# Optimization experiments

Measured on AMD Instinct MI355X. Metric: run time of the kernel, lower is better.

The kernel has to match this reference:

```python
import jax, jax.numpy as jnp
import numpy as np

NUM_HEADS = 8
HEAD_SIZE = 64
N_EMBEDS = 512


def setup_inputs() -> dict:
    key = jax.random.key(0)
    kx, kq, kk, kv, kw, kb = jax.random.split(key, 6)
    B, T, C = 8, 2048, N_EMBEDS
    H, D = NUM_HEADS, HEAD_SIZE
    s = 1.0 / np.sqrt(C)
    x = jax.random.normal(kx, (B, T, C), dtype=jnp.float32)
    Wq = jax.random.normal(kq, (H, C, D), dtype=jnp.float32) * s
    Wk = jax.random.normal(kk, (H, C, D), dtype=jnp.float32) * s
    Wv = jax.random.normal(kv, (H, C, D), dtype=jnp.float32) * s
    Wproj = jax.random.normal(kw, (H * D, C), dtype=jnp.float32) * (1.0 / np.sqrt(H * D))
    bproj = jnp.zeros((C,), dtype=jnp.float32)
    return {"x": x, "Wq": Wq, "Wk": Wk, "Wv": Wv, "Wproj": Wproj, "bproj": bproj}


def reference(x, Wq, Wk, Wv, Wproj, bproj):
    # x: [B,T,C]; Wq/Wk/Wv: [H,C,D]; Wproj: [H*D,C]; bproj: [C]
    B, T, C = x.shape
    H, _, D = Wq.shape
    scale = D ** -0.5
    q = jnp.einsum('btc,hcd->bhtd', x, Wq)
    k = jnp.einsum('btc,hcd->bhtd', x, Wk)
    v = jnp.einsum('btc,hcd->bhtd', x, Wv)
    scores = jnp.einsum('bhtd,bhsd->bhts', q, k) * scale  # [B,H,T,T]
    causal = jnp.tril(jnp.ones((T, T), dtype=bool))
    scores = jnp.where(causal, scores, -jnp.inf)
    weights = jax.nn.softmax(scores, axis=-1)  # dropout inactive at inference
    out = jnp.einsum('bhts,bhsd->bhtd', weights, v)  # [B,H,T,D]
    out = out.transpose(0, 2, 1, 3).reshape(B, T, H * D)  # concat heads
    return out @ Wproj + bproj
```

## Files before the change

### kernel.cpp

```cpp
#include <hip/hip_runtime.h>
#include <stdint.h>


typedef __attribute__((ext_vector_type(8))) short bf16x8;
typedef __attribute__((ext_vector_type(4))) float f32x4;
typedef unsigned short ushort_t;

#define MFMA16(a, b, c) __builtin_amdgcn_mfma_f32_16x16x32_bf16(a, b, c, 0, 0, 0)

__device__ __forceinline__ ushort_t f2bf(float x) {
    union { float f; uint32_t u; } v; v.f = x;
    uint32_t r = v.u + 0x7fffu + ((v.u >> 16) & 1u);
    return (ushort_t)(r >> 16);
}

__device__ __forceinline__ void gload_lds16(const void* g, void* l) {
    __builtin_amdgcn_global_load_lds(
        (const __attribute__((address_space(1))) unsigned int*)g,
        (__attribute__((address_space(3))) unsigned int*)l, 16, 0, 0);
}

__global__ __launch_bounds__(256) void k_convert_x(const float* __restrict__ x,
                                                   ushort_t* __restrict__ xb) {
    const size_t n = (size_t)8 * 2048 * 512;
    const size_t stride = (size_t)gridDim.x * 256 * 4;
    for (size_t i = ((size_t)blockIdx.x * 256 + threadIdx.x) * 4; i < n; i += stride) {
        float4 f = *(const float4*)(x + i);
        uint2 o;
        o.x = (uint32_t)f2bf(f.x) | ((uint32_t)f2bf(f.y) << 16);
        o.y = (uint32_t)f2bf(f.z) | ((uint32_t)f2bf(f.w) << 16);
        *(uint2*)(xb + i) = o;
    }
}

__global__ __launch_bounds__(256) void k_convert_w(const float* __restrict__ Wq,
                                                   const float* __restrict__ Wk,
                                                   const float* __restrict__ Wv,
                                                   const float* __restrict__ Wp,
                                                   ushort_t* __restrict__ wqkv,
                                                   ushort_t* __restrict__ wp) {
    int i = blockIdx.x * 256 + threadIdx.x;
    if (i < 3 * 512 * 512) {
        int which = i >> 18;
        int r = i & 262143;
        int n = r >> 9, k = r & 511;
        int h = n >> 6, d = n & 63;
        const float* W = which == 0 ? Wq : (which == 1 ? Wk : Wv);
        float val = W[((size_t)h * 512 + k) * 64 + d];
        if (which == 0) val *= 0.125f;
        wqkv[i] = f2bf(val);
    } else {
        int r = i - 3 * 512 * 512;
        int n = r >> 9, k = r & 511;
        wp[r] = f2bf(Wp[(size_t)k * 512 + n]);
    }
}

template <int KDIM>
__device__ __forceinline__ void gemm_tile_128(const ushort_t* __restrict__ A,
                                              const ushort_t* __restrict__ Bt,
                                              int m0, int n0,
                                              ushort_t* As, ushort_t* Bs,
                                              f32x4 (&acc)[4][4]) {
    const int tid = threadIdx.x;
    const int wave = tid >> 6, lane = tid & 63;
    const int wm = (wave >> 1) * 64, wn = (wave & 1) * 64;
    for (int k0 = 0; k0 < KDIM; k0 += 64) {
        __syncthreads();
#pragma unroll
        for (int i = 0; i < 4; i++) {
            int base = wave * 4096 + i * 1024;
            int bb = base + lane * 16;
            int row = bb >> 7;
            int sub = (bb >> 4) & 7;
            int swz = (sub ^ (row & 7)) << 4;
            gload_lds16((const char*)(A + (size_t)(m0 + row) * KDIM + k0) + swz,
                        (char*)As + base);
        }
#pragma unroll
        for (int i = 0; i < 4; i++) {
            int base = wave * 4096 + i * 1024;
            int bb = base + lane * 16;
            int row = bb >> 7;
            int sub = (bb >> 4) & 7;
            int swz = (sub ^ (row & 7)) << 4;
            gload_lds16((const char*)(Bt + (size_t)(n0 + row) * KDIM + k0) + swz,
                        (char*)Bs + base);
        }
        __syncthreads();
        bf16x8 af[4][2], bf[4][2];
#pragma unroll
        for (int mt = 0; mt < 4; mt++)
#pragma unroll
            for (int ks = 0; ks < 2; ks++) {
                int row = wm + mt * 16 + (lane & 15);
                int sub = ks * 4 + (lane >> 4);
                af[mt][ks] = *(const bf16x8*)((const char*)As + row * 128 +
                                              ((sub ^ (row & 7)) << 4));
            }
#pragma unroll
        for (int nt = 0; nt < 4; nt++)
#pragma unroll
            for (int ks = 0; ks < 2; ks++) {
                int row = wn + nt * 16 + (lane & 15);
                int sub = ks * 4 + (lane >> 4);
                bf[nt][ks] = *(const bf16x8*)((const char*)Bs + row * 128 +
                                              ((sub ^ (row & 7)) << 4));
            }
#pragma unroll
        for (int mt = 0; mt < 4; mt++)
#pragma unroll
            for (int nt = 0; nt < 4; nt++)
#pragma unroll
                for (int ks = 0; ks < 2; ks++)
                    acc[mt][nt] = MFMA16(af[mt][ks], bf[nt][ks], acc[mt][nt]);
    }
}

__global__ __launch_bounds__(256) void k_gemm_qkv(const ushort_t* __restrict__ xb,
                                                  const ushort_t* __restrict__ wqkv,
                                                  ushort_t* __restrict__ qo,
                                                  ushort_t* __restrict__ ko,
                                                  ushort_t* __restrict__ vo) {
    __shared__ __align__(16) ushort_t As[128 * 64];
    __shared__ __align__(16) ushort_t Bs[128 * 64];
    const int m0 = blockIdx.x * 128;
    const int n0g = blockIdx.y * 128;
    f32x4 acc[4][4] = {};
    gemm_tile_128<512>(xb, wqkv, m0, n0g, As, Bs, acc);
    const int tid = threadIdx.x, wave = tid >> 6, lane = tid & 63;
    const int wm = (wave >> 1) * 64, wn = (wave & 1) * 64;
    const int which = n0g >> 9;
    ushort_t* outp = which == 0 ? qo : (which == 1 ? ko : vo);
    const int n0 = n0g & 511;
#pragma unroll
    for (int mt = 0; mt < 4; mt++)
#pragma unroll
        for (int nt = 0; nt < 4; nt++)
#pragma unroll
            for (int e = 0; e < 4; e++) {
                int m = m0 + wm + mt * 16 + (lane >> 4) * 4 + e;
                int n = n0 + wn + nt * 16 + (lane & 15);
                int b = m >> 11, t = m & 2047;
                int h = n >> 6, d = n & 63;
                outp[((((size_t)b * 8 + h) * 2048 + t) << 6) + d] = f2bf(acc[mt][nt][e]);
            }
}

__global__ __launch_bounds__(256) void k_flash(const ushort_t* __restrict__ qp,
                                               const ushort_t* __restrict__ kp,
                                               const ushort_t* __restrict__ vp,
                                               ushort_t* __restrict__ attn) {
    __shared__ __align__(16) ushort_t Ks[64 * 64];
    __shared__ __align__(16) ushort_t Vt[64 * 72];
    __shared__ __align__(16) ushort_t Pl[4][16 * 72];
    const int bh = blockIdx.y;
    const int tid = threadIdx.x, wave = tid >> 6, lane = tid & 63;
    const size_t bh_off = (size_t)bh * 2048 * 64;
    const int b_ = bh >> 3, h_ = bh & 7;

    for (int p = 0; p < 2; ++p) {
        const int qb = (p == 0) ? blockIdx.x : (31 - blockIdx.x);
        const int qw0 = qb * 64 + wave * 16;

        bf16x8 qa[2];
        {
            const ushort_t* qrow = qp + bh_off + (size_t)(qw0 + (lane & 15)) * 64;
            qa[0] = *(const bf16x8*)(qrow + (lane >> 4) * 8);
            qa[1] = *(const bf16x8*)(qrow + 32 + (lane >> 4) * 8);
        }
        f32x4 o[4] = {};
        float m_run[4] = {-1e30f, -1e30f, -1e30f, -1e30f};
        float l_run[4] = {0.f, 0.f, 0.f, 0.f};

        for (int kb = 0; kb <= qb; ++kb) {
            const int kbase = kb * 64;
            __syncthreads();
#pragma unroll
            for (int i = 0; i < 2; i++) {
                int base = wave * 2048 + i * 1024;
                int bb = base + lane * 16;
                int row = bb >> 7;
                int sub = (bb >> 4) & 7;
                gload_lds16((const char*)(kp + bh_off + (size_t)(kbase + row) * 64) +
                                ((sub ^ (row & 7)) << 4),
                            (char*)Ks + base);
            }
#pragma unroll
            for (int it = 0; it < 2; ++it) {
                int t2 = tid + it * 256;
                int j = t2 >> 3;
                int mm = t2 & 7;
                int d0 = mm * 8;
                bf16x8 vv = *(const bf16x8*)(vp + bh_off + (size_t)(kbase + j) * 64 + d0);
#pragma unroll
                for (int e = 0; e < 8; e++) {
                    int ee = (e + mm) & 7;
                    Vt[(d0 + ee) * 72 + j] = (ushort_t)vv[ee];
                }
            }
            __syncthreads();
            f32x4 s[4];
#pragma unroll
            for (int kt = 0; kt < 4; kt++) {
                f32x4 z = {};
#pragma unroll
                for (int ds = 0; ds < 2; ++ds) {
                    int row = kt * 16 + (lane & 15);
                    int sub = ds * 4 + (lane >> 4);
                    bf16x8 kf = *(const bf16x8*)((const char*)Ks + row * 128 +
                                                 ((sub ^ (row & 7)) << 4));
                    z = MFMA16(qa[ds], kf, z);
                }
                s[kt] = z;
            }
            if (kb == qb) {
#pragma unroll
                for (int kt = 0; kt < 4; kt++)
#pragma unroll
                    for (int e = 0; e < 4; e++) {
                        int key = kbase + kt * 16 + (lane & 15);
                        int qq = qw0 + (lane >> 4) * 4 + e;
                        if (key > qq) s[kt][e] = -1e30f;
                    }
            }
            float pv[4][4];
#pragma unroll
            for (int e = 0; e < 4; e++) {
                float mx = fmaxf(fmaxf(s[0][e], s[1][e]), fmaxf(s[2][e], s[3][e]));
                mx = fmaxf(mx, __shfl_xor(mx, 1));
                mx = fmaxf(mx, __shfl_xor(mx, 2));
                mx = fmaxf(mx, __shfl_xor(mx, 4));
                mx = fmaxf(mx, __shfl_xor(mx, 8));
                float mn = fmaxf(m_run[e], mx);
                float alpha = __expf(m_run[e] - mn);
                float rs = 0.f;
#pragma unroll
                for (int kt = 0; kt < 4; kt++) {
                    float pp = __expf(s[kt][e] - mn);
                    pv[e][kt] = pp;
                    rs += pp;
                }
                rs += __shfl_xor(rs, 1);
                rs += __shfl_xor(rs, 2);
                rs += __shfl_xor(rs, 4);
                rs += __shfl_xor(rs, 8);
                l_run[e] = l_run[e] * alpha + rs;
                m_run[e] = mn;
#pragma unroll
                for (int dt = 0; dt < 4; dt++) o[dt][e] *= alpha;
            }
            ushort_t* pw = &Pl[wave][0];
#pragma unroll
            for (int e = 0; e < 4; e++) {
                int row = (lane >> 4) * 4 + e;
#pragma unroll
                for (int kt = 0; kt < 4; kt++)
                    pw[row * 72 + kt * 16 + (lane & 15)] = f2bf(pv[e][kt]);
            }
            asm volatile("s_waitcnt lgkmcnt(0)" ::: "memory");
            __builtin_amdgcn_sched_barrier(0);
            bf16x8 pa[2];
#pragma unroll
            for (int ks = 0; ks < 2; ks++)
                pa[ks] = *(const bf16x8*)(pw + (lane & 15) * 72 + ks * 32 + (lane >> 4) * 8);
#pragma unroll
            for (int dt = 0; dt < 4; dt++) {
                int drow = dt * 16 + (lane & 15);
#pragma unroll
                for (int ks = 0; ks < 2; ks++) {
                    bf16x8 vf = *(const bf16x8*)(Vt + drow * 72 + ks * 32 + (lane >> 4) * 8);
                    o[dt] = MFMA16(pa[ks], vf, o[dt]);
                }
            }
        }
#pragma unroll
        for (int e = 0; e < 4; e++) {
            float inv = 1.0f / l_run[e];
            int t = qw0 + (lane >> 4) * 4 + e;
            ushort_t* orow = attn + ((size_t)(b_ * 2048 + t) * 512) + h_ * 64;
#pragma unroll
            for (int dt = 0; dt < 4; dt++)
                orow[dt * 16 + (lane & 15)] = f2bf(o[dt][e] * inv);
        }
    }
}

__global__ __launch_bounds__(256) void k_gemm_proj(const ushort_t* __restrict__ attn,
                                                   const ushort_t* __restrict__ wp,
                                                   const float* __restrict__ bias,
                                                   float* __restrict__ out) {
    __shared__ __align__(16) ushort_t As[128 * 64];
    __shared__ __align__(16) ushort_t Bs[128 * 64];
    const int m0 = blockIdx.x * 128;
    const int n0 = blockIdx.y * 128;
    f32x4 acc[4][4] = {};
    gemm_tile_128<512>(attn, wp, m0, n0, As, Bs, acc);
    const int tid = threadIdx.x, wave = tid >> 6, lane = tid & 63;
    const int wm = (wave >> 1) * 64, wn = (wave & 1) * 64;
#pragma unroll
    for (int mt = 0; mt < 4; mt++)
#pragma unroll
        for (int nt = 0; nt < 4; nt++)
#pragma unroll
            for (int e = 0; e < 4; e++) {
                int m = m0 + wm + mt * 16 + (lane >> 4) * 4 + e;
                int n = n0 + wn + nt * 16 + (lane & 15);
                out[(size_t)m * 512 + n] = acc[mt][nt][e] + bias[n];
            }
}

extern "C" void kernel_launch(void* const* d_in, const int* in_sizes, int n_in,
                              void* d_out, int out_size, void* d_ws, size_t ws_size,
                              hipStream_t stream) {
    const float* x = (const float*)d_in[0];
    const float* Wq = (const float*)d_in[1];
    const float* Wk = (const float*)d_in[2];
    const float* Wv = (const float*)d_in[3];
    const float* Wp = (const float*)d_in[4];
    const float* bp = (const float*)d_in[5];
    float* out = (float*)d_out;

    ushort_t* ws = (ushort_t*)d_ws;
    const size_t NX = (size_t)8 * 2048 * 512;
    ushort_t* xb = ws;
    ushort_t* wqkv = xb + NX;
    ushort_t* wpj = wqkv + (size_t)3 * 512 * 512;
    ushort_t* q = wpj + (size_t)512 * 512;
    ushort_t* k = q + NX;
    ushort_t* v = k + NX;
    ushort_t* attn = xb;

    hipLaunchKernelGGL(k_convert_x, dim3(4096), dim3(256), 0, stream, x, xb);
    hipLaunchKernelGGL(k_convert_w, dim3(4096), dim3(256), 0, stream, Wq, Wk, Wv, Wp, wqkv, wpj);
    hipLaunchKernelGGL(k_gemm_qkv, dim3(128, 12), dim3(256), 0, stream, xb, wqkv, q, k, v);
    hipLaunchKernelGGL(k_flash, dim3(16, 64), dim3(256), 0, stream, q, k, v, attn);
    hipLaunchKernelGGL(k_gemm_proj, dim3(128, 4), dim3(256), 0, stream, attn, wpj, bp, out);
}
```

Baseline: 307.8 us.

## Compute transposed scores so P stays in registers, skipping LDS round-trip

The flash kernel swaps MFMA operand order to compute S^T, so each lane holds one query's scores across keys. K rows are permuted with a matching swizzle so the score registers line up directly with the A-operand layout for the PV MFMA, which removes the per-wave LDS P buffer, its stores and reloads, and the waitcnt barrier. Softmax now needs only two cross-lane shuffles per reduction instead of four per row. BF16 packing uses the hardware v_cvt_pk_bf16_f32 instruction, and outputs are written as packed 8-byte stores. The bf16 rounding in the hardware conversion may differ slightly from the manual rounding it replaces.

```diff
diff --git a/kernel.cpp b/kernel.cpp
--- a/kernel.cpp
+++ b/kernel.cpp
@@ -12,6 +12,12 @@
     union { float f; uint32_t u; } v; v.f = x;
     uint32_t r = v.u + 0x7fffu + ((v.u >> 16) & 1u);
     return (ushort_t)(r >> 16);
+}
+
+__device__ __forceinline__ uint32_t cvtpk_bf16(float lo, float hi) {
+    uint32_t r;
+    asm("v_cvt_pk_bf16_f32 %0, %1, %2" : "=v"(r) : "v"(lo), "v"(hi));
+    return r;
 }
 
 __device__ __forceinline__ void gload_lds16(const void* g, void* l) {
@@ -153,25 +159,25 @@
                                                ushort_t* __restrict__ attn) {
     __shared__ __align__(16) ushort_t Ks[64 * 64];
     __shared__ __align__(16) ushort_t Vt[64 * 72];
-    __shared__ __align__(16) ushort_t Pl[4][16 * 72];
     const int bh = blockIdx.y;
     const int tid = threadIdx.x, wave = tid >> 6, lane = tid & 63;
+    const int mq = lane & 15, g = lane >> 4;
     const size_t bh_off = (size_t)bh * 2048 * 64;
     const int b_ = bh >> 3, h_ = bh & 7;
 
     for (int p = 0; p < 2; ++p) {
         const int qb = (p == 0) ? blockIdx.x : (31 - blockIdx.x);
         const int qw0 = qb * 64 + wave * 16;
+        const int qq = qw0 + mq;
 
         bf16x8 qa[2];
         {
-            const ushort_t* qrow = qp + bh_off + (size_t)(qw0 + (lane & 15)) * 64;
-            qa[0] = *(const bf16x8*)(qrow + (lane >> 4) * 8);
-            qa[1] = *(const bf16x8*)(qrow + 32 + (lane >> 4) * 8);
+            const ushort_t* qrow = qp + bh_off + (size_t)qq * 64;
+            qa[0] = *(const bf16x8*)(qrow + g * 8);
+            qa[1] = *(const bf16x8*)(qrow + 32 + g * 8);
         }
         f32x4 o[4] = {};
-        float m_run[4] = {-1e30f, -1e30f, -1e30f, -1e30f};
-        float l_run[4] = {0.f, 0.f, 0.f, 0.f};
+        float m_run = -1e30f, l_run = 0.f;
 
         for (int kb = 0; kb <= qb; ++kb) {
             const int kbase = kb * 64;
@@ -182,8 +188,9 @@
                 int bb = base + lane * 16;
                 int row = bb >> 7;
                 int sub = (bb >> 4) & 7;
+                int frow = (((row >> 3) & 3) << 1) | (row & 1);
                 gload_lds16((const char*)(kp + bh_off + (size_t)(kbase + row) * 64) +
-                                ((sub ^ (row & 7)) << 4),
+                                ((sub ^ frow) << 4),
                             (char*)Ks + base);
             }
 #pragma unroll
@@ -202,86 +209,80 @@
             __syncthreads();
             f32x4 s[4];
 #pragma unroll
-            for (int kt = 0; kt < 4; kt++) {
+            for (int t = 0; t < 4; t++) {
+                int rs = ((t >> 1) << 5) + ((mq >> 2) << 3) + ((t & 1) << 2) + (mq & 3);
+                int ft = (((rs >> 3) & 3) << 1) | (rs & 1);
                 f32x4 z = {};
 #pragma unroll
                 for (int ds = 0; ds < 2; ++ds) {
-                    int row = kt * 16 + (lane & 15);
-                    int sub = ds * 4 + (lane >> 4);
-                    bf16x8 kf = *(const bf16x8*)((const char*)Ks + row * 128 +
-                                                 ((sub ^ (row & 7)) << 4));
-                    z = MFMA16(qa[ds], kf, z);
+                    bf16x8 kf = *(const bf16x8*)((const char*)Ks + rs * 128 +
+                                                 (((ds * 4 + g) ^ ft) << 4));
+                    z = MFMA16(kf, qa[ds], z);
                 }
-                s[kt] = z;
+                s[t] = z;
             }
             if (kb == qb) {
 #pragma unroll
-                for (int kt = 0; kt < 4; kt++)
+                for (int t = 0; t < 4; t++)
 #pragma unroll
                     for (int e = 0; e < 4; e++) {
-                        int key = kbase + kt * 16 + (lane & 15);
-                        int qq = qw0 + (lane >> 4) * 4 + e;
-                        if (key > qq) s[kt][e] = -1e30f;
+                        int key = kbase + ((t >> 1) << 5) + (g << 3) + ((t & 1) << 2) + e;
+                        if (key > qq) s[t][e] = -1e30f;
                     }
             }
-            float pv[4][4];
-#pragma unroll
-            for (int e = 0; e < 4; e++) {
-                float mx = fmaxf(fmaxf(s[0][e], s[1][e]), fmaxf(s[2][e], s[3][e]));
-                mx = fmaxf(mx, __shfl_xor(mx, 1));
-                mx = fmaxf(mx, __shfl_xor(mx, 2));
-                mx = fmaxf(mx, __shfl_xor(mx, 4));
-                mx = fmaxf(mx, __shfl_xor(mx, 8));
-                float mn = fmaxf(m_run[e], mx);
-                float alpha = __expf(m_run[e] - mn);
-                float rs = 0.f;
-#pragma unroll
-                for (int kt = 0; kt < 4; kt++) {
-                    float pp = __expf(s[kt][e] - mn);
-                    pv[e][kt] = pp;
-                    rs += pp;
+            float mx = s[0][0];
+#pragma unroll
+            for (int t = 0; t < 4; t++)
+#pragma unroll
+                for (int e = 0; e < 4; e++) mx = fmaxf(mx, s[t][e]);
+            mx = fmaxf(mx, __shfl_xor(mx, 16));
+            mx = fmaxf(mx, __shfl_xor(mx, 32));
+            float mn = fmaxf(m_run, mx);
+            float alpha = __expf(m_run - mn);
+            float pr[4][4];
+            float rs_ = 0.f;
+#pragma unroll
+            for (int t = 0; t < 4; t++)
+#pragma unroll
+                for (int e = 0; e < 4; e++) {
+                    float pp = __expf(s[t][e] - mn);
+                    pr[t][e] = pp;
+                    rs_ += pp;
                 }
-                rs += __shfl_xor(rs, 1);
-                rs += __shfl_xor(rs, 2);
-                rs += __shfl_xor(rs, 4);
-                rs += __shfl_xor(rs, 8);
-                l_run[e] = l_run[e] * alpha + rs;
-                m_run[e] = mn;
-#pragma unroll
-                for (int dt = 0; dt < 4; dt++) o[dt][e] *= alpha;
-            }
-            ushort_t* pw = &Pl[wave][0];
-#pragma unroll
-            for (int e = 0; e < 4; e++) {
-                int row = (lane >> 4) * 4 + e;
-#pragma unroll
-                for (int kt = 0; kt < 4; kt++)
-                    pw[row * 72 + kt * 16 + (lane & 15)] = f2bf(pv[e][kt]);
-            }
-            asm volatile("s_waitcnt lgkmcnt(0)" ::: "memory");
-            __builtin_amdgcn_sched_barrier(0);
-            bf16x8 pa[2];
-#pragma unroll
-            for (int ks = 0; ks < 2; ks++)
-                pa[ks] = *(const bf16x8*)(pw + (lane & 15) * 72 + ks * 32 + (lane >> 4) * 8);
+            rs_ += __shfl_xor(rs_, 16);
+            rs_ += __shfl_xor(rs_, 32);
+            l_run = l_run * alpha + rs_;
+            m_run = mn;
+#pragma unroll
+            for (int dt = 0; dt < 4; dt++)
+#pragma unroll
+                for (int e = 0; e < 4; e++) o[dt][e] *= alpha;
+            union { bf16x8 v; uint32_t u[4]; } pb[2];
+#pragma unroll
+            for (int ks = 0; ks < 2; ks++) {
+                pb[ks].u[0] = cvtpk_bf16(pr[2 * ks][0], pr[2 * ks][1]);
+                pb[ks].u[1] = cvtpk_bf16(pr[2 * ks][2], pr[2 * ks][3]);
+                pb[ks].u[2] = cvtpk_bf16(pr[2 * ks + 1][0], pr[2 * ks + 1][1]);
+                pb[ks].u[3] = cvtpk_bf16(pr[2 * ks + 1][2], pr[2 * ks + 1][3]);
+            }
 #pragma unroll
             for (int dt = 0; dt < 4; dt++) {
-                int drow = dt * 16 + (lane & 15);
+                int drow = dt * 16 + mq;
 #pragma unroll
                 for (int ks = 0; ks < 2; ks++) {
-                    bf16x8 vf = *(const bf16x8*)(Vt + drow * 72 + ks * 32 + (lane >> 4) * 8);
-                    o[dt] = MFMA16(pa[ks], vf, o[dt]);
+                    bf16x8 vf = *(const bf16x8*)(Vt + drow * 72 + ks * 32 + g * 8);
+                    o[dt] = MFMA16(vf, pb[ks].v, o[dt]);
                 }
             }
         }
-#pragma unroll
-        for (int e = 0; e < 4; e++) {
-            float inv = 1.0f / l_run[e];
-            int t = qw0 + (lane >> 4) * 4 + e;
-            ushort_t* orow = attn + ((size_t)(b_ * 2048 + t) * 512) + h_ * 64;
-#pragma unroll
-            for (int dt = 0; dt < 4; dt++)
-                orow[dt * 16 + (lane & 15)] = f2bf(o[dt][e] * inv);
+        float inv = 1.0f / l_run;
+        ushort_t* orow = attn + ((size_t)(b_ * 2048 + qq) * 512) + h_ * 64;
+#pragma unroll
+        for (int dt = 0; dt < 4; dt++) {
+            uint2 st;
+            st.x = cvtpk_bf16(o[dt][0] * inv, o[dt][1] * inv);
+            st.y = cvtpk_bf16(o[dt][2] * inv, o[dt][3] * inv);
+            *(uint2*)(orow + dt * 16 + g * 4) = st;
         }
     }
 }
```

Measured after the change: 247.2 us. -19.7%, faster.
